# Kernel tuning notes

Hardware: AMD Instinct MI355X
Metric: run time of the kernel (lower is better)

## Reference

```python
import jax, jax.numpy as jnp
import numpy as np
import math

EMBED_DIM = 1024
NUM_HEADS = 16
HEAD_DIM = EMBED_DIM // NUM_HEADS  # 64
MAX_SEQ_LEN = 2048


def rope_tables(max_seq_len, dim):
    pos = jnp.arange(max_seq_len, dtype=jnp.float32)
    div_term = jnp.exp(jnp.arange(0, dim, 2, dtype=jnp.float32) * -(math.log(10000.0) / dim))
    ang = pos[:, None] * div_term[None, :]  # [S, dim//2]
    return jnp.sin(ang), jnp.cos(ang)


def apply_rope(x, sin, cos):
    # x: [B, H, S, D]; sin/cos: [max_seq, D//2]
    S = x.shape[2]
    sin = sin[:S][None, None]  # [1,1,S,D//2]
    cos = cos[:S][None, None]
    x1, x2 = jnp.split(x, 2, axis=-1)
    return jnp.concatenate([cos * x1 - sin * x2, sin * x1 + cos * x2], axis=-1)


def setup_inputs() -> dict:
    key = jax.random.key(0)
    ks = jax.random.split(key, 5)
    B, S, E = 4, 2048, EMBED_DIM
    std = 1.0 / math.sqrt(E)
    x = jax.random.normal(ks[0], (B, S, E), dtype=jnp.float32)
    Wq = jax.random.normal(ks[1], (E, E), dtype=jnp.float32) * std
    Wk = jax.random.normal(ks[2], (E, E), dtype=jnp.float32) * std
    Wv = jax.random.normal(ks[3], (E, E), dtype=jnp.float32) * std
    Wo = jax.random.normal(ks[4], (E, E), dtype=jnp.float32) * std
    return {"x": x, "Wq": Wq, "Wk": Wk, "Wv": Wv, "Wo": Wo}


def reference(x, Wq, Wk, Wv, Wo):
    B, S, E = x.shape
    H, D = NUM_HEADS, HEAD_DIM
    scale = 1.0 / math.sqrt(D)
    sin, cos = rope_tables(MAX_SEQ_LEN, D)

    def split_heads(t):
        return t.reshape(B, S, H, D).transpose(0, 2, 1, 3)  # [B,H,S,D]

    q = split_heads(x @ Wq)
    k = split_heads(x @ Wk)
    v = split_heads(x @ Wv)
    q = apply_rope(q, sin, cos)
    k = apply_rope(k, sin, cos)

    scores = jnp.einsum('bhqd,bhkd->bhqk', q, k) * scale
    causal = jnp.where(jnp.tril(jnp.ones((S, S), dtype=bool)), 0.0, -1e9)
    scores = scores + causal[None, None]
    attn = jax.nn.softmax(scores, axis=-1)
    out = jnp.einsum('bhqk,bhkd->bhqd', attn, v)  # [B,H,S,D]
    out = out.transpose(0, 2, 1, 3).reshape(B, S, E)
    return out @ Wo
```

## Files before the change

kernel.cpp:

```cpp
#include <hip/hip_runtime.h>

#define DEVFN __device__ __forceinline__

typedef __attribute__((ext_vector_type(8))) short bf16x8;
typedef __attribute__((ext_vector_type(4))) float f32x4;
typedef __attribute__((ext_vector_type(16))) float f32x16;

#define MFMA16(a, b, c) __builtin_amdgcn_mfma_f32_16x16x32_bf16(a, b, c, 0, 0, 0)
#define MFMA32(a, b, c) __builtin_amdgcn_mfma_f32_32x32x16_bf16(a, b, c, 0, 0, 0)

DEVFN unsigned short f2bf(float f) {
  union { float f; unsigned u; } v; v.f = f;
  unsigned r = v.u + 0x7FFFu + ((v.u >> 16) & 1u);
  return (unsigned short)(r >> 16);
}
DEVFN unsigned pack2bf(float a, float b) {
  return (unsigned)f2bf(a) | ((unsigned)f2bf(b) << 16);
}
DEVFN unsigned cvtpk(float lo, float hi) {
  unsigned r;
  asm("v_cvt_pk_bf16_f32 %0, %1, %2" : "=v"(r) : "v"(lo), "v"(hi));
  return r;
}
DEVFN void pl32swap(unsigned& a, unsigned& b) {
  asm("v_permlane32_swap_b32 %0, %1" : "+v"(a), "+v"(b));
}
DEVFN void gll16(const void* g, void* l) {
  __builtin_amdgcn_global_load_lds((__attribute__((address_space(1))) void*)g,
                                   (__attribute__((address_space(3))) void*)l,
                                   16, 0, 0);
}


__global__ __launch_bounds__(256) void conv_x_k(const float* __restrict__ x,
                                                unsigned short* __restrict__ xb) {
  int i = (blockIdx.x * 256 + threadIdx.x) * 4;
  float4 v = *(const float4*)(x + i);
  uint2 u;
  u.x = pack2bf(v.x, v.y);
  u.y = pack2bf(v.z, v.w);
  *(uint2*)(xb + i) = u;
}

__global__ __launch_bounds__(256) void transp_k(
    const float* __restrict__ Wq, const float* __restrict__ Wk,
    const float* __restrict__ Wv, const float* __restrict__ Wo,
    unsigned short* __restrict__ Tq, unsigned short* __restrict__ Tk,
    unsigned short* __restrict__ Tv, unsigned short* __restrict__ To) {
  __shared__ unsigned short t[64 * 65];
  int z = blockIdx.z;
  const float* src = (z == 0) ? Wq : (z == 1) ? Wk : (z == 2) ? Wv : Wo;
  unsigned short* dst = (z == 0) ? Tq : (z == 1) ? Tk : (z == 2) ? Tv : To;
  int k0 = blockIdx.x * 64, n0 = blockIdx.y * 64;
  int tid = threadIdx.x;
#pragma unroll
  for (int i = 0; i < 16; ++i) {
    int flat = i * 256 + tid;
    int r = flat >> 6, cc = flat & 63;
    t[cc * 65 + r] = f2bf(src[(size_t)(k0 + r) * 1024 + n0 + cc]);
  }
  __syncthreads();
#pragma unroll
  for (int i = 0; i < 16; ++i) {
    int flat = i * 256 + tid;
    int rr = flat >> 6, cc = flat & 63;
    dst[(size_t)(n0 + rr) * 1024 + k0 + cc] = t[rr * 65 + cc];
  }
}

__global__ __launch_bounds__(256) void rope_k(float2* __restrict__ rtab) {
  int idx = blockIdx.x * 256 + threadIdx.x;
  int s = idx >> 5, j = idx & 31;
  float freq = expf(-0.28782313714981824f * (float)j);
  float ang = (float)s * freq;
  rtab[idx] = make_float2(sinf(ang), cosf(ang));
}

template <int MODE>
__global__ __launch_bounds__(256) void gemm_k(
    const unsigned short* __restrict__ A, const unsigned short* __restrict__ WT,
    void* __restrict__ outp, const float2* __restrict__ rtab) {
  __shared__ unsigned short At[128 * 64];
  __shared__ unsigned short Bt[128 * 64];
  const int tid = threadIdx.x;
  const int w = tid >> 6, lane = tid & 63, g = lane >> 4, c = lane & 15;
  const int wr = w >> 1, wc = w & 1;
  const int m0 = blockIdx.x * 128, n0 = blockIdx.y * 128;

  f32x4 zero = {0.f, 0.f, 0.f, 0.f};
  f32x4 acc[4][4];
#pragma unroll
  for (int i = 0; i < 4; ++i)
#pragma unroll
    for (int j = 0; j < 4; ++j) acc[i][j] = zero;

  for (int k0 = 0; k0 < 1024; k0 += 64) {
#pragma unroll
    for (int p = 0; p < 4; ++p) {
      int i = p * 256 + tid;
      int row = i >> 3, ls = i & 7;
      size_t off = ((size_t)(m0 + row) * 1024 + k0) * 2 + ((ls ^ (row & 7)) << 4);
      gll16((const char*)A + off, (char*)At + p * 4096 + w * 1024);
      size_t offb = ((size_t)(n0 + row) * 1024 + k0) * 2 + ((ls ^ (row & 7)) << 4);
      gll16((const char*)WT + offb, (char*)Bt + p * 4096 + w * 1024);
    }
    __syncthreads();
#pragma unroll
    for (int ks = 0; ks < 2; ++ks) {
      bf16x8 af[4], bfv[4];
#pragma unroll
      for (int am = 0; am < 4; ++am) {
        int row = wr * 64 + am * 16 + c;
        af[am] = *(const bf16x8*)(At + row * 64 + ((((ks << 2) | g) ^ (row & 7)) << 3));
      }
#pragma unroll
      for (int bn = 0; bn < 4; ++bn) {
        int row = wc * 64 + bn * 16 + c;
        bfv[bn] = *(const bf16x8*)(Bt + row * 64 + ((((ks << 2) | g) ^ (row & 7)) << 3));
      }
#pragma unroll
      for (int am = 0; am < 4; ++am)
#pragma unroll
        for (int bn = 0; bn < 4; ++bn)
          acc[am][bn] = MFMA16(af[am], bfv[bn], acc[am][bn]);
    }
    __syncthreads();
  }

  if (MODE == 0) {
    unsigned short* outb = (unsigned short*)outp;
#pragma unroll
    for (int am = 0; am < 4; ++am)
#pragma unroll
      for (int bp = 0; bp < 2; ++bp) {
        int col = n0 + wc * 64 + bp * 16 + c;
        int h = col >> 6, j = col & 63;
#pragma unroll
        for (int r = 0; r < 4; ++r) {
          int row = m0 + wr * 64 + am * 16 + (g << 2) + r;
          int b = row >> 11, s = row & 2047;
          float x1 = acc[am][bp][r], x2 = acc[am][bp + 2][r];
          float2 sc = rtab[s * 32 + j];
          float o1 = (sc.y * x1 - sc.x * x2) * 0.18033688011112042f;
          float o2 = (sc.x * x1 + sc.y * x2) * 0.18033688011112042f;
          size_t base = (((size_t)(b * 16 + h)) * 2048 + s) * 64;
          outb[base + j] = f2bf(o1);
          outb[base + 32 + j] = f2bf(o2);
        }
      }
  } else if (MODE == 1) {
    unsigned short* outb = (unsigned short*)outp;
#pragma unroll
    for (int am = 0; am < 4; ++am)
#pragma unroll
      for (int bp = 0; bp < 2; ++bp) {
        int col = n0 + wc * 64 + bp * 16 + c;
        int h = col >> 6, j = col & 63;
        const int kb = j >> 4, hil = (j >> 3) & 1, el = j & 7;
#pragma unroll
        for (int r = 0; r < 4; ++r) {
          int row = m0 + wr * 64 + am * 16 + (g << 2) + r;
          int b = row >> 11, s = row & 2047;
          float x1 = acc[am][bp][r], x2 = acc[am][bp + 2][r];
          float2 sc = rtab[s * 32 + j];
          float o1 = sc.y * x1 - sc.x * x2;
          float o2 = sc.x * x1 + sc.y * x2;
          size_t base = (size_t)(b * 16 + h) * 131072 + (size_t)(s >> 5) * 2048 +
                        (hil * 32 + (s & 31)) * 8 + el;
          outb[base + kb * 512] = f2bf(o1);
          outb[base + (kb + 2) * 512] = f2bf(o2);
        }
      }
  } else if (MODE == 2) {
    unsigned short* outb = (unsigned short*)outp;
#pragma unroll
    for (int am = 0; am < 4; ++am)
#pragma unroll
      for (int bn = 0; bn < 4; ++bn) {
        int col = n0 + wc * 64 + bn * 16 + c;
        int h = col >> 6, d = col & 63;
        int row0 = m0 + wr * 64 + am * 16 + (g << 2);
        int b = row0 >> 11, s0 = row0 & 2047;
        uint2 u;
        u.x = pack2bf(acc[am][bn][0], acc[am][bn][1]);
        u.y = pack2bf(acc[am][bn][2], acc[am][bn][3]);
        size_t off = (size_t)(b * 16 + h) * 131072 + (size_t)(s0 >> 6) * 4096 +
                     ((s0 >> 4) & 3) * 1024 + (d >> 5) * 512 +
                     (((s0 >> 3) & 1) * 32 + (d & 31)) * 8 + (s0 & 7);
        *(uint2*)(outb + off) = u;
      }
  } else {
    float* outf = (float*)outp;
#pragma unroll
    for (int am = 0; am < 4; ++am)
#pragma unroll
      for (int bn = 0; bn < 4; ++bn)
#pragma unroll
        for (int r = 0; r < 4; ++r)
          outf[(size_t)(m0 + wr * 64 + am * 16 + (g << 2) + r) * 1024 +
               (n0 + wc * 64 + bn * 16 + c)] = acc[am][bn][r];
  }
}

__global__ __launch_bounds__(256, 2) void attn_k(
    const unsigned short* __restrict__ Q, const unsigned short* __restrict__ Kf,
    const unsigned short* __restrict__ Vf, unsigned short* __restrict__ ctx) {
  const int blk = blockIdx.x;
  const int xcd = blk & 7, idx = blk >> 3;
  const int bh = (xcd << 3) + (idx & 7);
  const int pbase = (idx >> 3) << 2;
  const int tid = threadIdx.x;
  const int w = tid >> 6, lane = tid & 63;
  const int hi = lane >> 5, c5 = lane & 31;
  const int P = pbase + w;

  const unsigned short* Qbh = Q + (size_t)bh * 2048 * 64;
  const unsigned short* Kbh = Kf + (size_t)bh * 131072;
  const unsigned short* Vbh = Vf + (size_t)bh * 131072;
  const int b = bh >> 4, h = bh & 15;

  f32x16 zacc;
#pragma unroll
  for (int i = 0; i < 16; ++i) zacc[i] = 0.f;

  auto pass = [&](int U) {
    const int qw = U * 32;
    const int S = (U >> 1) + 1;

    bf16x8 qf[4];
#pragma unroll
    for (int kb = 0; kb < 4; ++kb)
      qf[kb] = *(const bf16x8*)(Qbh + (size_t)(qw + c5) * 64 + kb * 16 + hi * 8);

    f32x16 oacc[2];
    oacc[0] = zacc; oacc[1] = zacc;
    float m_run = -1e30f, l_run = 0.f;

    bf16x8 kfc[2][4];
#pragma unroll
    for (int t = 0; t < 2; ++t)
#pragma unroll
      for (int kb = 0; kb < 4; ++kb)
        kfc[t][kb] = *(const bf16x8*)(Kbh + t * 2048 + kb * 512 + lane * 8);

    for (int st = 0; st < S; ++st) {
      f32x16 sacc[2];
      __builtin_amdgcn_s_setprio(1);
#pragma unroll
      for (int t = 0; t < 2; ++t) {
        sacc[t] = MFMA32(kfc[t][0], qf[0], zacc);
#pragma unroll
        for (int kb = 1; kb < 4; ++kb)
          sacc[t] = MFMA32(kfc[t][kb], qf[kb], sacc[t]);
      }
      __builtin_amdgcn_s_setprio(0);

      bf16x8 vfr[2][4];
#pragma unroll
      for (int kb = 0; kb < 4; ++kb)
#pragma unroll
        for (int dt = 0; dt < 2; ++dt)
          vfr[dt][kb] = *(const bf16x8*)(Vbh + (size_t)st * 4096 + kb * 1024 +
                                         dt * 512 + lane * 8);
      bf16x8 kfn[2][4];
      if (st + 1 < S) {
#pragma unroll
        for (int t = 0; t < 2; ++t)
#pragma unroll
          for (int kb = 0; kb < 4; ++kb)
            kfn[t][kb] = *(const bf16x8*)(Kbh + (size_t)(st + 1) * 4096 +
                                          t * 2048 + kb * 512 + lane * 8);
      }

      if (st == S - 1) {
        const int q = qw + c5;
#pragma unroll
        for (int t = 0; t < 2; ++t) {
          const int kvb = st * 64 + t * 32 + (hi << 2);
#pragma unroll
          for (int i = 0; i < 16; ++i) {
            int kv = kvb + (i & 3) + ((i >> 2) << 3);
            if (kv > q) sacc[t][i] = -1e30f;
          }
        }
      }

      float vmax = fmaxf(sacc[0][0], sacc[0][1]);
#pragma unroll
      for (int t = 0; t < 2; ++t)
#pragma unroll
        for (int i = (t == 0 ? 2 : 0); i < 16; i += 2)
          vmax = fmaxf(vmax, fmaxf(sacc[t][i], sacc[t][i + 1]));
      vmax = fmaxf(vmax, __shfl_xor(vmax, 32, 64));
      if (!__all(vmax <= m_run + 8.0f)) {
        float m_new = fmaxf(m_run, vmax);
        float alpha = exp2f(m_run - m_new);
        l_run *= alpha;
#pragma unroll
        for (int i = 0; i < 16; ++i) {
          oacc[0][i] *= alpha;
          oacc[1][i] *= alpha;
        }
        m_run = m_new;
      }
      float psum = 0.f;
#pragma unroll
      for (int t = 0; t < 2; ++t)
#pragma unroll
        for (int i = 0; i < 16; ++i) {
          float pv = exp2f(sacc[t][i] - m_run);
          sacc[t][i] = pv;
          psum += pv;
        }
      psum += __shfl_xor(psum, 32, 64);
      l_run += psum;

      unsigned pword[4][4];
#pragma unroll
      for (int t = 0; t < 2; ++t) {
        unsigned X[4][2];
#pragma unroll
        for (int u = 0; u < 4; ++u)
#pragma unroll
          for (int wp = 0; wp < 2; ++wp)
            X[u][wp] = cvtpk(sacc[t][u * 4 + 2 * wp], sacc[t][u * 4 + 2 * wp + 1]);
#pragma unroll
        for (int par = 0; par < 2; ++par) {
          const int kb = 2 * t + par;
#pragma unroll
          for (int wp = 0; wp < 2; ++wp) {
            unsigned a = X[2 * par][wp], b2 = X[2 * par + 1][wp];
            pl32swap(a, b2);
            pword[kb][wp] = a;
            pword[kb][wp + 2] = b2;
          }
        }
      }

      __builtin_amdgcn_s_setprio(1);
#pragma unroll
      for (int kb = 0; kb < 4; ++kb) {
        union { unsigned u[4]; bf16x8 v; } pw;
#pragma unroll
        for (int k2 = 0; k2 < 4; ++k2) pw.u[k2] = pword[kb][k2];
        oacc[0] = MFMA32(vfr[0][kb], pw.v, oacc[0]);
        oacc[1] = MFMA32(vfr[1][kb], pw.v, oacc[1]);
      }
      __builtin_amdgcn_s_setprio(0);

      if (st + 1 < S) {
#pragma unroll
        for (int t = 0; t < 2; ++t)
#pragma unroll
          for (int kb = 0; kb < 4; ++kb) kfc[t][kb] = kfn[t][kb];
      }
    }

    const float linv = 1.f / l_run;
    unsigned short* crow = ctx + ((size_t)(b * 2048 + qw + c5)) * 1024 + h * 64;
#pragma unroll
    for (int dt = 0; dt < 2; ++dt)
#pragma unroll
      for (int u = 0; u < 4; ++u) {
        int d0 = dt * 32 + 8 * u + 4 * hi;
        uint2 o;
        o.x = cvtpk(oacc[dt][4 * u] * linv, oacc[dt][4 * u + 1] * linv);
        o.y = cvtpk(oacc[dt][4 * u + 2] * linv, oacc[dt][4 * u + 3] * linv);
        *(uint2*)(crow + d0) = o;
      }
  };

  pass(P);
  pass(63 - P);
}


extern "C" void kernel_launch(void* const* d_in, const int* in_sizes, int n_in,
                              void* d_out, int out_size, void* d_ws, size_t ws_size,
                              hipStream_t stream) {
  (void)in_sizes; (void)n_in; (void)out_size; (void)ws_size;
  const float* x = (const float*)d_in[0];
  const float* Wq = (const float*)d_in[1];
  const float* Wk = (const float*)d_in[2];
  const float* Wv = (const float*)d_in[3];
  const float* Wo = (const float*)d_in[4];
  char* ws = (char*)d_ws;
  const size_t MiB = 1024 * 1024;
  unsigned short* xb  = (unsigned short*)(ws);
  unsigned short* WTq = (unsigned short*)(ws + 16 * MiB);
  unsigned short* WTk = (unsigned short*)(ws + 18 * MiB);
  unsigned short* WTv = (unsigned short*)(ws + 20 * MiB);
  unsigned short* WTo = (unsigned short*)(ws + 22 * MiB);
  unsigned short* Qb  = (unsigned short*)(ws + 24 * MiB);
  unsigned short* Kfb = (unsigned short*)(ws + 40 * MiB);
  unsigned short* Vfb = (unsigned short*)(ws + 56 * MiB);
  unsigned short* ctx = (unsigned short*)(ws + 72 * MiB);
  float2* rtab = (float2*)(ws + 88 * MiB);

  conv_x_k<<<8192, 256, 0, stream>>>(x, xb);
  transp_k<<<dim3(16, 16, 4), 256, 0, stream>>>(Wq, Wk, Wv, Wo, WTq, WTk, WTv, WTo);
  rope_k<<<256, 256, 0, stream>>>(rtab);
  gemm_k<0><<<dim3(64, 8), 256, 0, stream>>>(xb, WTq, Qb, rtab);
  gemm_k<1><<<dim3(64, 8), 256, 0, stream>>>(xb, WTk, Kfb, rtab);
  gemm_k<2><<<dim3(64, 8), 256, 0, stream>>>(xb, WTv, Vfb, rtab);
  attn_k<<<512, 256, 0, stream>>>(Qb, Kfb, Vfb, ctx);
  gemm_k<3><<<dim3(64, 8), 256, 0, stream>>>(ctx, WTo, d_out, rtab);
}
```

Measured before the change: 184.6 us.

## Split attention KV range across wave pairs with LDS softmax merge

Each query tile's KV loop is now split in half between two waves (split-K style), and the partial outputs are merged through shared memory using log-sum-exp rescaling. The grid is doubled to 1024 blocks and launch bounds are raised to 4 blocks per CU to increase parallelism and shorten per-wave critical paths. The K register double-buffer prefetch is dropped in favour of direct loads inside the loop. The exchange adds LDS traffic, a block barrier, and bf16 rounding of the partial outputs before the merge, which may cost some accuracy.

New measurement: 197.2 us. 6.8% more time.

```diff
diff --git a/kernel.cpp b/kernel.cpp
--- a/kernel.cpp
+++ b/kernel.cpp
@@ -202,17 +202,21 @@
   }
 }
 
-__global__ __launch_bounds__(256, 2) void attn_k(
+__global__ __launch_bounds__(256, 4) void attn_k(
     const unsigned short* __restrict__ Q, const unsigned short* __restrict__ Kf,
     const unsigned short* __restrict__ Vf, unsigned short* __restrict__ ctx) {
+  __shared__ unsigned smem[2 * 3 * 64 * 19];
+
   const int blk = blockIdx.x;
-  const int xcd = blk & 7, idx = blk >> 3;
-  const int bh = (xcd << 3) + (idx & 7);
-  const int pbase = (idx >> 3) << 2;
+  const int xcd = blk & 7, r = blk >> 3;
+  const int bh = (xcd << 3) + (r & 7);
+  const int p2 = r >> 3;
   const int tid = threadIdx.x;
   const int w = tid >> 6, lane = tid & 63;
   const int hi = lane >> 5, c5 = lane & 31;
-  const int P = pbase + w;
+  const int P = p2 * 2 + (w >> 1);
+  const int role = w & 1;
+  const int base = (w >> 1) * 3;
 
   const unsigned short* Qbh = Q + (size_t)bh * 2048 * 64;
   const unsigned short* Kbh = Kf + (size_t)bh * 131072;
@@ -223,56 +227,42 @@
 #pragma unroll
   for (int i = 0; i < 16; ++i) zacc[i] = 0.f;
 
-  auto pass = [&](int U) {
-    const int qw = U * 32;
-    const int S = (U >> 1) + 1;
-
+  auto process = [&](int u, int s0, int s1, int dstp, float& m_run,
+                     float& l_run, f32x16 (&oacc)[2]) {
+    const int qw = u * 32;
     bf16x8 qf[4];
 #pragma unroll
     for (int kb = 0; kb < 4; ++kb)
       qf[kb] = *(const bf16x8*)(Qbh + (size_t)(qw + c5) * 64 + kb * 16 + hi * 8);
-
-    f32x16 oacc[2];
     oacc[0] = zacc; oacc[1] = zacc;
-    float m_run = -1e30f, l_run = 0.f;
-
-    bf16x8 kfc[2][4];
-#pragma unroll
-    for (int t = 0; t < 2; ++t)
-#pragma unroll
-      for (int kb = 0; kb < 4; ++kb)
-        kfc[t][kb] = *(const bf16x8*)(Kbh + t * 2048 + kb * 512 + lane * 8);
-
-    for (int st = 0; st < S; ++st) {
+    m_run = -1e30f; l_run = 0.f;
+
+    for (int st = s0; st < s1; ++st) {
       f32x16 sacc[2];
+      const unsigned short* kbase = Kbh + (size_t)st * 4096 + lane * 8;
       __builtin_amdgcn_s_setprio(1);
 #pragma unroll
       for (int t = 0; t < 2; ++t) {
-        sacc[t] = MFMA32(kfc[t][0], qf[0], zacc);
-#pragma unroll
-        for (int kb = 1; kb < 4; ++kb)
-          sacc[t] = MFMA32(kfc[t][kb], qf[kb], sacc[t]);
+        bf16x8 k0 = *(const bf16x8*)(kbase + t * 2048);
+        bf16x8 k1 = *(const bf16x8*)(kbase + t * 2048 + 512);
+        bf16x8 k2 = *(const bf16x8*)(kbase + t * 2048 + 1024);
+        bf16x8 k3 = *(const bf16x8*)(kbase + t * 2048 + 1536);
+        sacc[t] = MFMA32(k0, qf[0], zacc);
+        sacc[t] = MFMA32(k1, qf[1], sacc[t]);
+        sacc[t] = MFMA32(k2, qf[2], sacc[t]);
+        sacc[t] = MFMA32(k3, qf[3], sacc[t]);
       }
       __builtin_amdgcn_s_setprio(0);
 
+      const unsigned short* vbase = Vbh + (size_t)st * 4096 + lane * 8;
       bf16x8 vfr[2][4];
 #pragma unroll
-      for (int kb = 0; kb < 4; ++kb)
-#pragma unroll
-        for (int dt = 0; dt < 2; ++dt)
-          vfr[dt][kb] = *(const bf16x8*)(Vbh + (size_t)st * 4096 + kb * 1024 +
-                                         dt * 512 + lane * 8);
-      bf16x8 kfn[2][4];
-      if (st + 1 < S) {
-#pragma unroll
-        for (int t = 0; t < 2; ++t)
-#pragma unroll
-          for (int kb = 0; kb < 4; ++kb)
-            kfn[t][kb] = *(const bf16x8*)(Kbh + (size_t)(st + 1) * 4096 +
-                                          t * 2048 + kb * 512 + lane * 8);
-      }
-
-      if (st == S - 1) {
+      for (int kb = 0; kb < 4; ++kb) {
+        vfr[0][kb] = *(const bf16x8*)(vbase + kb * 1024);
+        vfr[1][kb] = *(const bf16x8*)(vbase + kb * 1024 + 512);
+      }
+
+      if (st == dstp) {
         const int q = qw + c5;
 #pragma unroll
         for (int t = 0; t < 2; ++t) {
@@ -320,10 +310,10 @@
       for (int t = 0; t < 2; ++t) {
         unsigned X[4][2];
 #pragma unroll
-        for (int u = 0; u < 4; ++u)
+        for (int u2 = 0; u2 < 4; ++u2)
 #pragma unroll
           for (int wp = 0; wp < 2; ++wp)
-            X[u][wp] = cvtpk(sacc[t][u * 4 + 2 * wp], sacc[t][u * 4 + 2 * wp + 1]);
+            X[u2][wp] = cvtpk(sacc[t][u2 * 4 + 2 * wp], sacc[t][u2 * 4 + 2 * wp + 1]);
 #pragma unroll
         for (int par = 0; par < 2; ++par) {
           const int kb = 2 * t + par;
@@ -347,31 +337,93 @@
         oacc[1] = MFMA32(vfr[1][kb], pw.v, oacc[1]);
       }
       __builtin_amdgcn_s_setprio(0);
-
-      if (st + 1 < S) {
-#pragma unroll
-        for (int t = 0; t < 2; ++t)
-#pragma unroll
-          for (int kb = 0; kb < 4; ++kb) kfc[t][kb] = kfn[t][kb];
-      }
     }
-
-    const float linv = 1.f / l_run;
-    unsigned short* crow = ctx + ((size_t)(b * 2048 + qw + c5)) * 1024 + h * 64;
+  };
+
+  auto store_partial = [&](int slot, const f32x16 (&o)[2], float m, float l) {
+    unsigned* p = smem + ((size_t)slot * 64 + lane) * 19;
 #pragma unroll
     for (int dt = 0; dt < 2; ++dt)
 #pragma unroll
-      for (int u = 0; u < 4; ++u) {
-        int d0 = dt * 32 + 8 * u + 4 * hi;
+      for (int idx = 0; idx < 8; ++idx)
+        p[dt * 8 + idx] = cvtpk(o[dt][2 * idx], o[dt][2 * idx + 1]);
+    p[16] = __float_as_uint(m);
+    p[17] = __float_as_uint(l);
+  };
+
+  auto bf_lo = [](unsigned u) { return __uint_as_float(u << 16); };
+  auto bf_hi = [](unsigned u) { return __uint_as_float(u & 0xFFFF0000u); };
+
+  auto merge_slots = [&](int s0, int s1, int u) {
+    const unsigned* q0 = smem + ((size_t)s0 * 64 + lane) * 19;
+    const unsigned* q1 = smem + ((size_t)s1 * 64 + lane) * 19;
+    float m0 = __uint_as_float(q0[16]), l0 = __uint_as_float(q0[17]);
+    float m1 = __uint_as_float(q1[16]), l1 = __uint_as_float(q1[17]);
+    float m = fmaxf(m0, m1);
+    float a0 = exp2f(m0 - m), a1 = exp2f(m1 - m);
+    float li = 1.f / (l0 * a0 + l1 * a1);
+    a0 *= li; a1 *= li;
+    unsigned short* crow = ctx + ((size_t)(b * 2048 + u * 32 + c5)) * 1024 + h * 64;
+#pragma unroll
+    for (int dt = 0; dt < 2; ++dt)
+#pragma unroll
+      for (int uu = 0; uu < 4; ++uu) {
+        unsigned w0a = q0[dt * 8 + 2 * uu], w1a = q1[dt * 8 + 2 * uu];
+        unsigned w0b = q0[dt * 8 + 2 * uu + 1], w1b = q1[dt * 8 + 2 * uu + 1];
         uint2 o;
-        o.x = cvtpk(oacc[dt][4 * u] * linv, oacc[dt][4 * u + 1] * linv);
-        o.y = cvtpk(oacc[dt][4 * u + 2] * linv, oacc[dt][4 * u + 3] * linv);
-        *(uint2*)(crow + d0) = o;
+        o.x = cvtpk(bf_lo(w0a) * a0 + bf_lo(w1a) * a1,
+                    bf_hi(w0a) * a0 + bf_hi(w1a) * a1);
+        o.y = cvtpk(bf_lo(w0b) * a0 + bf_lo(w1b) * a1,
+                    bf_hi(w0b) * a0 + bf_hi(w1b) * a1);
+        *(uint2*)(crow + dt * 32 + 8 * uu + 4 * hi) = o;
       }
   };
 
-  pass(P);
-  pass(63 - P);
+  auto merge_reg = [&](const f32x16 (&o)[2], float m_r, float l_r, int s0, int u) {
+    const unsigned* q0 = smem + ((size_t)s0 * 64 + lane) * 19;
+    float m0 = __uint_as_float(q0[16]), l0 = __uint_as_float(q0[17]);
+    float m = fmaxf(m0, m_r);
+    float a0 = exp2f(m0 - m), ar = exp2f(m_r - m);
+    float li = 1.f / (l0 * a0 + l_r * ar);
+    a0 *= li; ar *= li;
+    unsigned short* crow = ctx + ((size_t)(b * 2048 + u * 32 + c5)) * 1024 + h * 64;
+#pragma unroll
+    for (int dt = 0; dt < 2; ++dt)
+#pragma unroll
+      for (int uu = 0; uu < 4; ++uu) {
+        unsigned w0a = q0[dt * 8 + 2 * uu];
+        unsigned w0b = q0[dt * 8 + 2 * uu + 1];
+        uint2 ov;
+        ov.x = cvtpk(o[dt][4 * uu] * ar + bf_lo(w0a) * a0,
+                     o[dt][4 * uu + 1] * ar + bf_hi(w0a) * a0);
+        ov.y = cvtpk(o[dt][4 * uu + 2] * ar + bf_lo(w0b) * a0,
+                     o[dt][4 * uu + 3] * ar + bf_hi(w0b) * a0);
+        *(uint2*)(crow + dt * 32 + 8 * uu + 4 * hi) = ov;
+      }
+  };
+
+  const int V = 63 - P;
+  const int Sa = (P >> 1) + 1, Sb = (V >> 1) + 1;
+  const int ha = Sa >> 1, hb = Sb >> 1;
+
+  float m, l;
+  f32x16 oacc[2];
+  if (role == 0) {
+    process(P, 0, ha, -1, m, l, oacc);
+    store_partial(base + 0, oacc, m, l);
+    process(V, 0, hb, -1, m, l, oacc);
+    store_partial(base + 2, oacc, m, l);
+  } else {
+    process(P, ha, Sa, Sa - 1, m, l, oacc);
+    store_partial(base + 1, oacc, m, l);
+    process(V, hb, Sb, Sb - 1, m, l, oacc);
+  }
+  __syncthreads();
+  if (role == 0) {
+    merge_slots(base + 0, base + 1, P);
+  } else {
+    merge_reg(oacc, m, l, base + 2, V);
+  }
 }
 
 
@@ -403,6 +455,6 @@
   gemm_k<0><<<dim3(64, 8), 256, 0, stream>>>(xb, WTq, Qb, rtab);
   gemm_k<1><<<dim3(64, 8), 256, 0, stream>>>(xb, WTk, Kfb, rtab);
   gemm_k<2><<<dim3(64, 8), 256, 0, stream>>>(xb, WTv, Vfb, rtab);
-  attn_k<<<512, 256, 0, stream>>>(Qb, Kfb, Vfb, ctx);
+  attn_k<<<1024, 256, 0, stream>>>(Qb, Kfb, Vfb, ctx);
   gemm_k<3><<<dim3(64, 8), 256, 0, stream>>>(ctx, WTo, d_out, rtab);
 }
```
